# Kernel optimization log

Measured on AMD Instinct MI355X. Metric: run time of the kernel, lower is better.

## Reference

```python
import jax, jax.numpy as jnp
import numpy as np

B, D, U = 32768, 256, 256
P0, P1, NC = 128, 64, 1


def setup_inputs() -> dict:
    key = jax.random.key(0)
    ks = jax.random.split(key, 36)
    nrm = lambda k, shp, s=0.05: jax.random.normal(k, shp, jnp.float32) * s
    inp = {
        "x": jax.random.normal(ks[0], (B, D), jnp.float32),
        "click": jax.random.uniform(ks[1], (B, 1), dtype=jnp.float32),
        "h_c": jax.random.normal(ks[2], (B, U), jnp.float32),
        "h_v": jax.random.normal(ks[3], (B, U), jnp.float32),
        "s_c": jax.random.normal(ks[4], (B, U), jnp.float32),
        "s_v": jax.random.normal(ks[5], (B, U), jnp.float32),
        "g_prev": jax.random.randint(ks[6], (B, U), 0, 2).astype(jnp.int32),
        # gate weights: order [f, i, o, g]; x-gates have bias, h-gates do not
        "Wx_c": nrm(ks[7], (4, D, U)), "bx_c": nrm(ks[8], (4, U)), "Wh_c": nrm(ks[9], (4, U, U)),
        "Wx_v": nrm(ks[10], (4, D, U)), "bx_v": nrm(ks[11], (4, U)), "Wh_v": nrm(ks[12], (4, U, U)),
        "W_schat_c": nrm(ks[13], (U, U)), "W_schat_v": nrm(ks[14], (U, U)),
        "W_svhat_v": nrm(ks[15], (U, U)), "W_svhat_c": nrm(ks[16], (U, U)),
        "Wpc0": nrm(ks[17], (U, P0)), "bpc0": nrm(ks[18], (P0,)),
        "Wpc1": nrm(ks[19], (P0, P1)), "bpc1": nrm(ks[20], (P1,)),
        "Wfcc": nrm(ks[21], (P1, NC)), "bfcc": nrm(ks[22], (NC,)),
        "Wpv0": nrm(ks[23], (U, P0)), "bpv0": nrm(ks[24], (P0,)),
        "Wpv1": nrm(ks[25], (P0, P1)), "bpv1": nrm(ks[26], (P1,)),
        "Wfcv": nrm(ks[27], (P1, NC)), "bfcv": nrm(ks[28], (NC,)),
    }
    return inp


def _leaky(x):
    return jnp.where(x > 0, x, 0.3 * x)  # keras LeakyReLU default alpha=0.3


def _mlp(h, W0, b0, W1, b1, Wf, bf):
    a = _leaky(h @ W0 + b0)
    a = _leaky(a @ W1 + b1)
    return jax.nn.sigmoid(a @ Wf + bf)


def reference(x, click, h_c, h_v, s_c, s_v, g_prev,
              Wx_c, bx_c, Wh_c, Wx_v, bx_v, Wh_v,
              W_schat_c, W_schat_v, W_svhat_v, W_svhat_c,
              Wpc0, bpc0, Wpc1, bpc1, Wfcc, bfcc,
              Wpv0, bpv0, Wpv1, bpv1, Wfcv, bfcv):
    gp = g_prev > 0  # [B, U]
    # click branch
    s_c_hat = jnp.where(gp, h_v @ W_schat_v, h_c @ W_schat_c)
    pre_c = (jnp.einsum('bd,kdu->kbu', x, Wx_c) + bx_c[:, None, :]
             + jnp.einsum('bu,kuv->kbv', s_c_hat, Wh_c))  # [4, B, U]
    f_c = jax.nn.sigmoid(pre_c[0]); i_c = jax.nn.sigmoid(pre_c[1])
    o_c = jax.nn.sigmoid(pre_c[2]); g_c = jnp.tanh(pre_c[3])
    s_c_n = i_c * g_c + jnp.where(gp, 0.0, f_c * s_c)
    h_c_n = o_c * jnp.tanh(s_c_n)
    h_c_p = _mlp(h_c_n, Wpc0, bpc0, Wpc1, bpc1, Wfcc, bfcc)  # [B, 1]
    # conversion branch, gated by click label
    gm = click >= 0.5  # [B, 1] broadcasts over U (== tf.tile)
    s_v_hat = h_v @ W_svhat_v + jnp.where(gm, h_c_n @ W_svhat_c, 0.0)
    pre_v = (jnp.einsum('bd,kdu->kbu', x, Wx_v) + bx_v[:, None, :]
             + jnp.einsum('bu,kuv->kbv', s_v_hat, Wh_v))
    f_v = jax.nn.sigmoid(pre_v[0]); i_v = jax.nn.sigmoid(pre_v[1])
    o_v = jax.nn.sigmoid(pre_v[2]); g_v = jnp.tanh(pre_v[3])
    s_v_n = jnp.where(gm, f_v * s_v + i_v * g_v, s_v)
    h_v_n = jnp.where(gm, o_v * jnp.tanh(s_v_n), h_v)
    h_v_p = _mlp(h_v_n, Wpv0, bpv0, Wpv1, bpv1, Wfcv, bfcv) * h_c_p
    g_new = jnp.broadcast_to(gm.astype(jnp.float32), (x.shape[0], U))
    return h_c_p, h_v_p, h_c_n, h_v_n, s_c_n, s_v_n, g_new
```

## Files before the change

kernel.cpp:

```cpp
#include <hip/hip_runtime.h>
#include <hip/hip_bf16.h>
#include <math.h>

typedef __bf16 bf16;
typedef __bf16 bf16x8 __attribute__((ext_vector_type(8)));
typedef float  f32x4  __attribute__((ext_vector_type(4)));

#define NB 32768
#define NU 256

#define MFMA(a,b,c) __builtin_amdgcn_mfma_f32_16x16x32_bf16((a),(b),(c),0,0,0)

static __device__ __forceinline__ float sigf(float x) {
    return 1.0f / (1.0f + __expf(-x));
}

static __device__ __forceinline__ void ld16(bf16* l, const bf16* g) {
    __builtin_amdgcn_global_load_lds(
        (const __attribute__((address_space(1))) void*)g,
        (__attribute__((address_space(3))) void*)l, 16, 0, 0);
}

static __device__ __forceinline__ bf16x8 frag(const bf16* buf, int row, int hi) {
    return *reinterpret_cast<const bf16x8*>(buf + row * 32 + hi * 8);
}

__global__ void k_cvt(const float* __restrict__ x, const float* __restrict__ h_v,
                      const float* __restrict__ h_c,
                      bf16* __restrict__ xs, bf16* __restrict__ hv_cat,
                      bf16* __restrict__ hcb)
{
    const int j = blockIdx.y;
    const int gid = blockIdx.x * 256 + threadIdx.x;
    const int row = gid >> 5, col = (gid & 31) * 8;
    const float* src = (j == 0) ? x : (j == 1) ? h_v : h_c;
    bf16* dst; int stride;
    if (j == 0)      { dst = xs;     stride = 512; }
    else if (j == 1) { dst = hv_cat; stride = 512; }
    else             { dst = hcb;    stride = 256; }
    const f32x4* s4 = reinterpret_cast<const f32x4*>(src + row * 256 + col);
    const f32x4 a = s4[0], b = s4[1];
    bf16x8 o;
    o[0] = (bf16)a[0]; o[1] = (bf16)a[1]; o[2] = (bf16)a[2]; o[3] = (bf16)a[3];
    o[4] = (bf16)b[0]; o[5] = (bf16)b[1]; o[6] = (bf16)b[2]; o[7] = (bf16)b[3];
    *reinterpret_cast<bf16x8*>(dst + row * stride + col) = o;
}

struct TrJobs {
    const float* src[24];
    bf16*        dst[24];
    int R[24], C[24], dstr[24];
};

__global__ void k_tr(TrJobs J) {
    __shared__ float tile[32][33];
    const int j = blockIdx.y;
    const int R = J.R[j], C = J.C[j], dstr = J.dstr[j];
    const int tilesC = C >> 5;
    const int tr = blockIdx.x / tilesC, tc = blockIdx.x % tilesC;
    if (tr >= (R >> 5)) return;
    const int r0 = tr * 32, c0 = tc * 32;
    const int tx = threadIdx.x, ty = threadIdx.y;
    const float* src = J.src[j];
    bf16* dst = J.dst[j];
#pragma unroll
    for (int i = 0; i < 4; ++i)
        tile[ty + 8 * i][tx] = src[(r0 + ty + 8 * i) * C + c0 + tx];
    __syncthreads();
#pragma unroll
    for (int i = 0; i < 4; ++i)
        dst[(c0 + ty + 8 * i) * dstr + r0 + tx] = (bf16)tile[tx][ty + 8 * i];
}

__global__ __launch_bounds__(256) void k_schat_t(
    const bf16* __restrict__ hc, const bf16* __restrict__ hvcat,
    const bf16* __restrict__ WTc, const bf16* __restrict__ WTv,
    const int* __restrict__ g_prev, bf16* __restrict__ xs)
{
    __shared__ bf16 A1[128 * 32], A2[128 * 32], B1[64 * 32], B2[64 * 32];
    const int tid = threadIdx.x, lane = tid & 63, w = tid >> 6;
    const int lr = lane & 15, hi = lane >> 4;
    const int r0 = blockIdx.x * 128, c0 = blockIdx.y * 64;
    const int wr = w >> 1, wc = w & 1;
    const int srow = tid >> 2, skc = (tid & 3) * 8;
    f32x4 acc1[4][2] = {}, acc2[4][2] = {};
    for (int kk = 0; kk < 8; ++kk) {
        const int k0 = kk * 32;
        if (kk) __syncthreads();
        ld16(A1 + tid * 8,        hc    + (r0 + srow) * 256 + k0 + skc);
        ld16(A1 + 2048 + tid * 8, hc    + (r0 + 64 + srow) * 256 + k0 + skc);
        ld16(A2 + tid * 8,        hvcat + (r0 + srow) * 512 + k0 + skc);
        ld16(A2 + 2048 + tid * 8, hvcat + (r0 + 64 + srow) * 512 + k0 + skc);
        ld16(B1 + tid * 8,        WTc   + (c0 + srow) * 256 + k0 + skc);
        ld16(B2 + tid * 8,        WTv   + (c0 + srow) * 256 + k0 + skc);
        __syncthreads();
        bf16x8 a1[4], a2[4], b1[2], b2[2];
#pragma unroll
        for (int i = 0; i < 4; ++i) {
            a1[i] = frag(A1, wr * 64 + i * 16 + lr, hi);
            a2[i] = frag(A2, wr * 64 + i * 16 + lr, hi);
        }
#pragma unroll
        for (int jj = 0; jj < 2; ++jj) {
            b1[jj] = frag(B1, wc * 32 + jj * 16 + lr, hi);
            b2[jj] = frag(B2, wc * 32 + jj * 16 + lr, hi);
        }
#pragma unroll
        for (int i = 0; i < 4; ++i)
#pragma unroll
            for (int jj = 0; jj < 2; ++jj) {
                acc1[i][jj] = MFMA(a1[i], b1[jj], acc1[i][jj]);
                acc2[i][jj] = MFMA(a2[i], b2[jj], acc2[i][jj]);
            }
    }
#pragma unroll
    for (int i = 0; i < 4; ++i)
#pragma unroll
        for (int jj = 0; jj < 2; ++jj)
#pragma unroll
            for (int r = 0; r < 4; ++r) {
                const int row = r0 + wr * 64 + i * 16 + hi * 4 + r;
                const int col = c0 + wc * 32 + jj * 16 + lr;
                const int o = row * 256 + col;
                const float v = (g_prev[o] > 0) ? acc2[i][jj][r] : acc1[i][jj][r];
                xs[row * 512 + 256 + col] = (bf16)v;
            }
}

__global__ __launch_bounds__(256) void k_svhat_t(
    const bf16* __restrict__ hvcat, const bf16* __restrict__ Wsv,
    bf16* __restrict__ xs)
{
    __shared__ bf16 A[128 * 32], B[128 * 32];
    const int tid = threadIdx.x, lane = tid & 63, w = tid >> 6;
    const int lr = lane & 15, hi = lane >> 4;
    const int r0 = blockIdx.x * 128, c0 = blockIdx.y * 128;
    const int wr = w >> 1, wc = w & 1;
    const int srow = tid >> 2, skc = (tid & 3) * 8;
    f32x4 acc[4][4] = {};
    for (int kk = 0; kk < 16; ++kk) {
        const int k0 = kk * 32;
        if (kk) __syncthreads();
        ld16(A + tid * 8,        hvcat + (r0 + srow) * 512 + k0 + skc);
        ld16(A + 2048 + tid * 8, hvcat + (r0 + 64 + srow) * 512 + k0 + skc);
        ld16(B + tid * 8,        Wsv   + (c0 + srow) * 512 + k0 + skc);
        ld16(B + 2048 + tid * 8, Wsv   + (c0 + 64 + srow) * 512 + k0 + skc);
        __syncthreads();
        bf16x8 a[4], b[4];
#pragma unroll
        for (int i = 0; i < 4; ++i) a[i] = frag(A, wr * 64 + i * 16 + lr, hi);
#pragma unroll
        for (int jj = 0; jj < 4; ++jj) b[jj] = frag(B, wc * 64 + jj * 16 + lr, hi);
#pragma unroll
        for (int i = 0; i < 4; ++i)
#pragma unroll
            for (int jj = 0; jj < 4; ++jj)
                acc[i][jj] = MFMA(a[i], b[jj], acc[i][jj]);
    }
#pragma unroll
    for (int i = 0; i < 4; ++i)
#pragma unroll
        for (int jj = 0; jj < 4; ++jj)
#pragma unroll
            for (int r = 0; r < 4; ++r) {
                const int row = r0 + wr * 64 + i * 16 + hi * 4 + r;
                const int col = c0 + wc * 64 + jj * 16 + lr;
                xs[row * 512 + 256 + col] = (bf16)acc[i][jj][r];
            }
}

__global__ __launch_bounds__(256) void k_gates_t(
    const bf16* __restrict__ xs, const bf16* __restrict__ WgT,
    const float* __restrict__ bx, const float* __restrict__ click,
    const int* __restrict__ g_prev, const float* __restrict__ s_prev,
    const float* __restrict__ h_prev,
    float* __restrict__ out_s, float* __restrict__ out_h,
    float* __restrict__ out_g, bf16* __restrict__ hnb,
    bf16* __restrict__ hmask_dst, int mode)
{
    __shared__ bf16 A[128 * 32], B[128 * 32];
    const int tid = threadIdx.x, lane = tid & 63, w = tid >> 6;
    const int lr = lane & 15, hi = lane >> 4;
    const int r0 = blockIdx.x * 128, u0 = blockIdx.y * 32;
    const int srow = tid >> 2, skc = (tid & 3) * 8;
    f32x4 acc[2][8] = {};
    for (int kk = 0; kk < 16; ++kk) {
        const int k0 = kk * 32;
        if (kk) __syncthreads();
        ld16(A + tid * 8,        xs + (r0 + srow) * 512 + k0 + skc);
        ld16(A + 2048 + tid * 8, xs + (r0 + 64 + srow) * 512 + k0 + skc);
        {
            int nl = srow, g = nl >> 5, ul = nl & 31;
            ld16(B + tid * 8, WgT + (g * 256 + u0 + ul) * 512 + k0 + skc);
            nl = 64 + srow; g = nl >> 5; ul = nl & 31;
            ld16(B + 2048 + tid * 8, WgT + (g * 256 + u0 + ul) * 512 + k0 + skc);
        }
        __syncthreads();
        bf16x8 a[2], b[8];
#pragma unroll
        for (int i = 0; i < 2; ++i) a[i] = frag(A, w * 32 + i * 16 + lr, hi);
#pragma unroll
        for (int nb = 0; nb < 8; ++nb) b[nb] = frag(B, nb * 16 + lr, hi);
#pragma unroll
        for (int i = 0; i < 2; ++i)
#pragma unroll
            for (int nb = 0; nb < 8; ++nb)
                acc[i][nb] = MFMA(a[i], b[nb], acc[i][nb]);
    }
#pragma unroll
    for (int uh = 0; uh < 2; ++uh) {
        const int u = u0 + uh * 16 + lr;
        const float bf_ = bx[u], bi_ = bx[256 + u];
        const float bo_ = bx[512 + u], bg_ = bx[768 + u];
#pragma unroll
        for (int i = 0; i < 2; ++i)
#pragma unroll
            for (int r = 0; r < 4; ++r) {
                const int row = r0 + w * 32 + i * 16 + hi * 4 + r;
                const int o = row * 256 + u;
                const float f  = sigf(acc[i][0 + uh][r] + bf_);
                const float ii = sigf(acc[i][2 + uh][r] + bi_);
                const float oo = sigf(acc[i][4 + uh][r] + bo_);
                const float gg = tanhf(acc[i][6 + uh][r] + bg_);
                if (mode == 0) {
                    const bool gp = g_prev[o] > 0;
                    const float sn = ii * gg + (gp ? 0.0f : f * s_prev[o]);
                    const float hn = oo * tanhf(sn);
                    out_s[o] = sn;
                    out_h[o] = hn;
                    hnb[o]   = (bf16)hn;
                    hmask_dst[row * 512 + 256 + u] =
                        (click[row] >= 0.5f) ? (bf16)hn : (bf16)0.0f;
                } else {
                    const bool m = click[row] >= 0.5f;
                    const float sv = s_prev[o];
                    const float sn = m ? (f * sv + ii * gg) : sv;
                    const float hn = m ? (oo * tanhf(sn)) : h_prev[o];
                    out_s[o] = sn;
                    out_h[o] = hn;
                    out_g[o] = m ? 1.0f : 0.0f;
                    hnb[o]   = (bf16)hn;
                }
            }
    }
}

__global__ __launch_bounds__(256) void k_mlp_t(
    const bf16* __restrict__ A_, int K, int ksteps,
    const bf16* __restrict__ WT, const float* __restrict__ bias,
    bf16* __restrict__ outp, int N)
{
    __shared__ bf16 A[128 * 32], B[64 * 32];
    const int tid = threadIdx.x, lane = tid & 63, w = tid >> 6;
    const int lr = lane & 15, hi = lane >> 4;
    const int r0 = blockIdx.x * 128, c0 = blockIdx.y * 64;
    const int srow = tid >> 2, skc = (tid & 3) * 8;
    f32x4 acc[2][4] = {};
    for (int kk = 0; kk < ksteps; ++kk) {
        const int k0 = kk * 32;
        if (kk) __syncthreads();
        ld16(A + tid * 8,        A_ + (r0 + srow) * K + k0 + skc);
        ld16(A + 2048 + tid * 8, A_ + (r0 + 64 + srow) * K + k0 + skc);
        ld16(B + tid * 8,        WT + (c0 + srow) * K + k0 + skc);
        __syncthreads();
        bf16x8 a[2], b[4];
#pragma unroll
        for (int i = 0; i < 2; ++i) a[i] = frag(A, w * 32 + i * 16 + lr, hi);
#pragma unroll
        for (int jj = 0; jj < 4; ++jj) b[jj] = frag(B, jj * 16 + lr, hi);
#pragma unroll
        for (int i = 0; i < 2; ++i)
#pragma unroll
            for (int jj = 0; jj < 4; ++jj)
                acc[i][jj] = MFMA(a[i], b[jj], acc[i][jj]);
    }
#pragma unroll
    for (int i = 0; i < 2; ++i)
#pragma unroll
        for (int jj = 0; jj < 4; ++jj)
#pragma unroll
            for (int r = 0; r < 4; ++r) {
                const int row = r0 + w * 32 + i * 16 + hi * 4 + r;
                const int col = c0 + jj * 16 + lr;
                float v = acc[i][jj][r] + bias[col];
                v = v > 0.0f ? v : 0.3f * v;
                outp[row * N + col] = (bf16)v;
            }
}

__global__ void k_final(
    const bf16* __restrict__ a2, const float* __restrict__ wv,
    const float* __restrict__ bias, const float* __restrict__ scale,
    float* __restrict__ outp)
{
    const int b = blockIdx.x * blockDim.x + threadIdx.x;
    const bf16x8* rp = reinterpret_cast<const bf16x8*>(a2 + b * 64);
    float s = bias[0];
#pragma unroll
    for (int j = 0; j < 8; ++j) {
        const bf16x8 f = rp[j];
#pragma unroll
        for (int e = 0; e < 8; ++e) s += (float)f[e] * wv[j * 8 + e];
    }
    float v = sigf(s);
    if (scale) v *= scale[b];
    outp[b] = v;
}

extern "C" void kernel_launch(void* const* d_in, const int* in_sizes, int n_in,
                              void* d_out, int out_size, void* d_ws, size_t ws_size,
                              hipStream_t stream)
{
    const float* x         = (const float*)d_in[0];
    const float* click     = (const float*)d_in[1];
    const float* h_c       = (const float*)d_in[2];
    const float* h_v       = (const float*)d_in[3];
    const float* s_c       = (const float*)d_in[4];
    const float* s_v       = (const float*)d_in[5];
    const int*   g_prev    = (const int*)d_in[6];
    const float* Wx_c      = (const float*)d_in[7];
    const float* bx_c      = (const float*)d_in[8];
    const float* Wh_c      = (const float*)d_in[9];
    const float* Wx_v      = (const float*)d_in[10];
    const float* bx_v      = (const float*)d_in[11];
    const float* Wh_v      = (const float*)d_in[12];
    const float* W_schat_c = (const float*)d_in[13];
    const float* W_schat_v = (const float*)d_in[14];
    const float* W_svhat_v = (const float*)d_in[15];
    const float* W_svhat_c = (const float*)d_in[16];
    const float* Wpc0 = (const float*)d_in[17];
    const float* bpc0 = (const float*)d_in[18];
    const float* Wpc1 = (const float*)d_in[19];
    const float* bpc1 = (const float*)d_in[20];
    const float* Wfcc = (const float*)d_in[21];
    const float* bfcc = (const float*)d_in[22];
    const float* Wpv0 = (const float*)d_in[23];
    const float* bpv0 = (const float*)d_in[24];
    const float* Wpv1 = (const float*)d_in[25];
    const float* bpv1 = (const float*)d_in[26];
    const float* Wfcv = (const float*)d_in[27];
    const float* bfcv = (const float*)d_in[28];

    float* out     = (float*)d_out;
    float* out_hcp = out;
    float* out_hvp = out + NB;
    float* out_hcn = out + 2 * NB;
    float* out_hvn = out_hcn + NB * NU;
    float* out_scn = out_hvn + NB * NU;
    float* out_svn = out_scn + NB * NU;
    float* out_gnw = out_svn + NB * NU;

    bf16* w = (bf16*)d_ws;
    bf16* WTc    = w; w += 256 * 256;
    bf16* WTv    = w; w += 256 * 256;
    bf16* Wsv    = w; w += 256 * 512;
    bf16* WT_pc0 = w; w += 128 * 256;
    bf16* WT_pv0 = w; w += 128 * 256;
    bf16* WT_pc1 = w; w += 64 * 128;
    bf16* WT_pv1 = w; w += 64 * 128;
    bf16* WgT_c  = w; w += 4 * 256 * 512;
    bf16* WgT_v  = w; w += 4 * 256 * 512;
    bf16* xs     = w; w += NB * 512;
    bf16* hv_cat = w; w += NB * 512;
    bf16* buf256 = w; w += NB * 256;
    bf16* bufP0  = w; w += NB * 128;
    bf16* bufP1  = w; w += NB * 64;

    TrJobs J;
    int j = 0;
    J.src[j] = W_schat_c; J.dst[j] = WTc; J.R[j] = 256; J.C[j] = 256; J.dstr[j] = 256; ++j;
    J.src[j] = W_schat_v; J.dst[j] = WTv; J.R[j] = 256; J.C[j] = 256; J.dstr[j] = 256; ++j;
    J.src[j] = W_svhat_v; J.dst[j] = Wsv;       J.R[j] = 256; J.C[j] = 256; J.dstr[j] = 512; ++j;
    J.src[j] = W_svhat_c; J.dst[j] = Wsv + 256; J.R[j] = 256; J.C[j] = 256; J.dstr[j] = 512; ++j;
    J.src[j] = Wpc0; J.dst[j] = WT_pc0; J.R[j] = 256; J.C[j] = 128; J.dstr[j] = 256; ++j;
    J.src[j] = Wpv0; J.dst[j] = WT_pv0; J.R[j] = 256; J.C[j] = 128; J.dstr[j] = 256; ++j;
    J.src[j] = Wpc1; J.dst[j] = WT_pc1; J.R[j] = 128; J.C[j] = 64;  J.dstr[j] = 128; ++j;
    J.src[j] = Wpv1; J.dst[j] = WT_pv1; J.R[j] = 128; J.C[j] = 64;  J.dstr[j] = 128; ++j;
    for (int g = 0; g < 4; ++g) {
        J.src[j] = Wx_c + g * 65536; J.dst[j] = WgT_c + g * 131072;       J.R[j] = 256; J.C[j] = 256; J.dstr[j] = 512; ++j;
        J.src[j] = Wh_c + g * 65536; J.dst[j] = WgT_c + g * 131072 + 256; J.R[j] = 256; J.C[j] = 256; J.dstr[j] = 512; ++j;
    }
    for (int g = 0; g < 4; ++g) {
        J.src[j] = Wx_v + g * 65536; J.dst[j] = WgT_v + g * 131072;       J.R[j] = 256; J.C[j] = 256; J.dstr[j] = 512; ++j;
        J.src[j] = Wh_v + g * 65536; J.dst[j] = WgT_v + g * 131072 + 256; J.R[j] = 256; J.C[j] = 256; J.dstr[j] = 512; ++j;
    }

    k_cvt<<<dim3(4096, 3), 256, 0, stream>>>(x, h_v, h_c, xs, hv_cat, buf256);
    k_tr<<<dim3(64, 24), dim3(32, 8), 0, stream>>>(J);

    k_schat_t<<<dim3(256, 4), 256, 0, stream>>>(buf256, hv_cat, WTc, WTv, g_prev, xs);
    k_gates_t<<<dim3(256, 8), 256, 0, stream>>>(xs, WgT_c, bx_c, click, g_prev, s_c,
                                                nullptr, out_scn, out_hcn, nullptr,
                                                buf256, hv_cat, 0);
    k_mlp_t<<<dim3(256, 2), 256, 0, stream>>>(buf256, 256, 8, WT_pc0, bpc0, bufP0, 128);
    k_mlp_t<<<dim3(256, 1), 256, 0, stream>>>(bufP0, 128, 4, WT_pc1, bpc1, bufP1, 64);
    k_final<<<NB / 256, 256, 0, stream>>>(bufP1, Wfcc, bfcc, nullptr, out_hcp);

    k_svhat_t<<<dim3(256, 2), 256, 0, stream>>>(hv_cat, Wsv, xs);
    k_gates_t<<<dim3(256, 8), 256, 0, stream>>>(xs, WgT_v, bx_v, click, nullptr, s_v,
                                                h_v, out_svn, out_hvn, out_gnw,
                                                buf256, nullptr, 1);
    k_mlp_t<<<dim3(256, 2), 256, 0, stream>>>(buf256, 256, 8, WT_pv0, bpv0, bufP0, 128);
    k_mlp_t<<<dim3(256, 1), 256, 0, stream>>>(bufP0, 128, 4, WT_pv1, bpv1, bufP1, 64);
    k_final<<<NB / 256, 256, 0, stream>>>(bufP1, Wfcv, bfcv, out_hcp, out_hvp);
}
```

Before: 681.1 us.

## Fuse MLP stages, bit-pack g_prev, widen K tiles with swizzled LDS, faster activations

Replaces the two-layer MLP plus final-dot kernels with one fused kernel per branch that keeps the hidden layer in shared memory, removing the intermediate bf16 buffers and extra launches. g_prev is packed into a bitmask once, so the gating kernels read bits instead of int32 per element. GEMM kernels now stage 64-wide K tiles with an XOR-swizzled LDS layout, halving barrier count and reducing bank conflicts. sigmoid uses a hardware reciprocal and tanh is computed through sigmoid, at some precision cost.

```diff
diff --git a/kernel.cpp b/kernel.cpp
--- a/kernel.cpp
+++ b/kernel.cpp
@@ -12,7 +12,10 @@
 #define MFMA(a,b,c) __builtin_amdgcn_mfma_f32_16x16x32_bf16((a),(b),(c),0,0,0)
 
 static __device__ __forceinline__ float sigf(float x) {
-    return 1.0f / (1.0f + __expf(-x));
+    return __builtin_amdgcn_rcpf(1.0f + __expf(-x));
+}
+static __device__ __forceinline__ float tanh_(float x) {
+    return fmaf(2.0f, sigf(2.0f * x), -1.0f);
 }
 
 static __device__ __forceinline__ void ld16(bf16* l, const bf16* g) {
@@ -21,8 +24,8 @@
         (__attribute__((address_space(3))) void*)l, 16, 0, 0);
 }
 
-static __device__ __forceinline__ bf16x8 frag(const bf16* buf, int row, int hi) {
-    return *reinterpret_cast<const bf16x8*>(buf + row * 32 + hi * 8);
+static __device__ __forceinline__ bf16x8 frag64(const bf16* buf, int row, int kc) {
+    return *reinterpret_cast<const bf16x8*>(buf + row * 64 + ((kc ^ (row & 7)) * 8));
 }
 
 __global__ void k_cvt(const float* __restrict__ x, const float* __restrict__ h_v,
@@ -46,6 +49,17 @@
     *reinterpret_cast<bf16x8*>(dst + row * stride + col) = o;
 }
 
+__global__ void k_pack(const int* __restrict__ g, unsigned long long* __restrict__ m)
+{
+    const int tid0 = blockIdx.x * 256 + threadIdx.x;
+#pragma unroll
+    for (int it = 0; it < 32; ++it) {
+        const int i = tid0 + it * (1024 * 256);
+        const unsigned long long b = __ballot(g[i] > 0);
+        if ((threadIdx.x & 63) == 0) m[i >> 6] = b;
+    }
+}
+
 struct TrJobs {
     const float* src[24];
     bf16*        dst[24];
@@ -75,43 +89,53 @@
 __global__ __launch_bounds__(256) void k_schat_t(
     const bf16* __restrict__ hc, const bf16* __restrict__ hvcat,
     const bf16* __restrict__ WTc, const bf16* __restrict__ WTv,
-    const int* __restrict__ g_prev, bf16* __restrict__ xs)
-{
-    __shared__ bf16 A1[128 * 32], A2[128 * 32], B1[64 * 32], B2[64 * 32];
+    const unsigned* __restrict__ gmask, bf16* __restrict__ xs)
+{
+    __shared__ bf16 A1[128 * 64], A2[128 * 64], B1[64 * 64], B2[64 * 64];
     const int tid = threadIdx.x, lane = tid & 63, w = tid >> 6;
     const int lr = lane & 15, hi = lane >> 4;
     const int r0 = blockIdx.x * 128, c0 = blockIdx.y * 64;
     const int wr = w >> 1, wc = w & 1;
-    const int srow = tid >> 2, skc = (tid & 3) * 8;
     f32x4 acc1[4][2] = {}, acc2[4][2] = {};
-    for (int kk = 0; kk < 8; ++kk) {
-        const int k0 = kk * 32;
+    for (int kk = 0; kk < 4; ++kk) {
+        const int k0 = kk * 64;
         if (kk) __syncthreads();
-        ld16(A1 + tid * 8,        hc    + (r0 + srow) * 256 + k0 + skc);
-        ld16(A1 + 2048 + tid * 8, hc    + (r0 + 64 + srow) * 256 + k0 + skc);
-        ld16(A2 + tid * 8,        hvcat + (r0 + srow) * 512 + k0 + skc);
-        ld16(A2 + 2048 + tid * 8, hvcat + (r0 + 64 + srow) * 512 + k0 + skc);
-        ld16(B1 + tid * 8,        WTc   + (c0 + srow) * 256 + k0 + skc);
-        ld16(B2 + tid * 8,        WTv   + (c0 + srow) * 256 + k0 + skc);
-        __syncthreads();
-        bf16x8 a1[4], a2[4], b1[2], b2[2];
-#pragma unroll
-        for (int i = 0; i < 4; ++i) {
-            a1[i] = frag(A1, wr * 64 + i * 16 + lr, hi);
-            a2[i] = frag(A2, wr * 64 + i * 16 + lr, hi);
-        }
-#pragma unroll
-        for (int jj = 0; jj < 2; ++jj) {
-            b1[jj] = frag(B1, wc * 32 + jj * 16 + lr, hi);
-            b2[jj] = frag(B2, wc * 32 + jj * 16 + lr, hi);
-        }
-#pragma unroll
-        for (int i = 0; i < 4; ++i)
+#pragma unroll
+        for (int p = 0; p < 4; ++p) {
+            const int t = tid + p * 256;
+            const int row = t >> 3, gs = ((t & 7) ^ (row & 7)) * 8;
+            ld16(A1 + t * 8, hc    + (r0 + row) * 256 + k0 + gs);
+            ld16(A2 + t * 8, hvcat + (r0 + row) * 512 + k0 + gs);
+        }
+#pragma unroll
+        for (int p = 0; p < 2; ++p) {
+            const int t = tid + p * 256;
+            const int row = t >> 3, gs = ((t & 7) ^ (row & 7)) * 8;
+            ld16(B1 + t * 8, WTc + (c0 + row) * 256 + k0 + gs);
+            ld16(B2 + t * 8, WTv + (c0 + row) * 256 + k0 + gs);
+        }
+        __syncthreads();
+#pragma unroll
+        for (int ks = 0; ks < 2; ++ks) {
+            bf16x8 a1[4], a2[4], b1[2], b2[2];
+#pragma unroll
+            for (int i = 0; i < 4; ++i) {
+                a1[i] = frag64(A1, wr * 64 + i * 16 + lr, ks * 4 + hi);
+                a2[i] = frag64(A2, wr * 64 + i * 16 + lr, ks * 4 + hi);
+            }
 #pragma unroll
             for (int jj = 0; jj < 2; ++jj) {
-                acc1[i][jj] = MFMA(a1[i], b1[jj], acc1[i][jj]);
-                acc2[i][jj] = MFMA(a2[i], b2[jj], acc2[i][jj]);
+                b1[jj] = frag64(B1, wc * 32 + jj * 16 + lr, ks * 4 + hi);
+                b2[jj] = frag64(B2, wc * 32 + jj * 16 + lr, ks * 4 + hi);
             }
+#pragma unroll
+            for (int i = 0; i < 4; ++i)
+#pragma unroll
+                for (int jj = 0; jj < 2; ++jj) {
+                    acc1[i][jj] = MFMA(a1[i], b1[jj], acc1[i][jj]);
+                    acc2[i][jj] = MFMA(a2[i], b2[jj], acc2[i][jj]);
+                }
+        }
     }
 #pragma unroll
     for (int i = 0; i < 4; ++i)
@@ -121,9 +145,8 @@
             for (int r = 0; r < 4; ++r) {
                 const int row = r0 + wr * 64 + i * 16 + hi * 4 + r;
                 const int col = c0 + wc * 32 + jj * 16 + lr;
-                const int o = row * 256 + col;
-                const float v = (g_prev[o] > 0) ? acc2[i][jj][r] : acc1[i][jj][r];
-                xs[row * 512 + 256 + col] = (bf16)v;
+                const bool gp = (gmask[row * 8 + (col >> 5)] >> (col & 31)) & 1;
+                xs[row * 512 + 256 + col] = (bf16)(gp ? acc2[i][jj][r] : acc1[i][jj][r]);
             }
 }
 
@@ -131,31 +154,36 @@
     const bf16* __restrict__ hvcat, const bf16* __restrict__ Wsv,
     bf16* __restrict__ xs)
 {
-    __shared__ bf16 A[128 * 32], B[128 * 32];
+    __shared__ bf16 A[128 * 64], B[128 * 64];
     const int tid = threadIdx.x, lane = tid & 63, w = tid >> 6;
     const int lr = lane & 15, hi = lane >> 4;
     const int r0 = blockIdx.x * 128, c0 = blockIdx.y * 128;
     const int wr = w >> 1, wc = w & 1;
-    const int srow = tid >> 2, skc = (tid & 3) * 8;
     f32x4 acc[4][4] = {};
-    for (int kk = 0; kk < 16; ++kk) {
-        const int k0 = kk * 32;
+    for (int kk = 0; kk < 8; ++kk) {
+        const int k0 = kk * 64;
         if (kk) __syncthreads();
-        ld16(A + tid * 8,        hvcat + (r0 + srow) * 512 + k0 + skc);
-        ld16(A + 2048 + tid * 8, hvcat + (r0 + 64 + srow) * 512 + k0 + skc);
-        ld16(B + tid * 8,        Wsv   + (c0 + srow) * 512 + k0 + skc);
-        ld16(B + 2048 + tid * 8, Wsv   + (c0 + 64 + srow) * 512 + k0 + skc);
-        __syncthreads();
-        bf16x8 a[4], b[4];
-#pragma unroll
-        for (int i = 0; i < 4; ++i) a[i] = frag(A, wr * 64 + i * 16 + lr, hi);
-#pragma unroll
-        for (int jj = 0; jj < 4; ++jj) b[jj] = frag(B, wc * 64 + jj * 16 + lr, hi);
-#pragma unroll
-        for (int i = 0; i < 4; ++i)
-#pragma unroll
-            for (int jj = 0; jj < 4; ++jj)
-                acc[i][jj] = MFMA(a[i], b[jj], acc[i][jj]);
+#pragma unroll
+        for (int p = 0; p < 4; ++p) {
+            const int t = tid + p * 256;
+            const int row = t >> 3, gs = ((t & 7) ^ (row & 7)) * 8;
+            ld16(A + t * 8, hvcat + (r0 + row) * 512 + k0 + gs);
+            ld16(B + t * 8, Wsv   + (c0 + row) * 512 + k0 + gs);
+        }
+        __syncthreads();
+#pragma unroll
+        for (int ks = 0; ks < 2; ++ks) {
+            bf16x8 a[4], b[4];
+#pragma unroll
+            for (int i = 0; i < 4; ++i) a[i] = frag64(A, wr * 64 + i * 16 + lr, ks * 4 + hi);
+#pragma unroll
+            for (int jj = 0; jj < 4; ++jj) b[jj] = frag64(B, wc * 64 + jj * 16 + lr, ks * 4 + hi);
+#pragma unroll
+            for (int i = 0; i < 4; ++i)
+#pragma unroll
+                for (int jj = 0; jj < 4; ++jj)
+                    acc[i][jj] = MFMA(a[i], b[jj], acc[i][jj]);
+        }
     }
 #pragma unroll
     for (int i = 0; i < 4; ++i)
@@ -172,139 +200,192 @@
 __global__ __launch_bounds__(256) void k_gates_t(
     const bf16* __restrict__ xs, const bf16* __restrict__ WgT,
     const float* __restrict__ bx, const float* __restrict__ click,
-    const int* __restrict__ g_prev, const float* __restrict__ s_prev,
+    const unsigned* __restrict__ gmask, const float* __restrict__ s_prev,
     const float* __restrict__ h_prev,
     float* __restrict__ out_s, float* __restrict__ out_h,
     float* __restrict__ out_g, bf16* __restrict__ hnb,
     bf16* __restrict__ hmask_dst, int mode)
 {
-    __shared__ bf16 A[128 * 32], B[128 * 32];
+    __shared__ bf16 A[128 * 64], B[128 * 64];
     const int tid = threadIdx.x, lane = tid & 63, w = tid >> 6;
     const int lr = lane & 15, hi = lane >> 4;
     const int r0 = blockIdx.x * 128, u0 = blockIdx.y * 32;
-    const int srow = tid >> 2, skc = (tid & 3) * 8;
     f32x4 acc[2][8] = {};
-    for (int kk = 0; kk < 16; ++kk) {
-        const int k0 = kk * 32;
+    for (int kk = 0; kk < 8; ++kk) {
+        const int k0 = kk * 64;
         if (kk) __syncthreads();
-        ld16(A + tid * 8,        xs + (r0 + srow) * 512 + k0 + skc);
-        ld16(A + 2048 + tid * 8, xs + (r0 + 64 + srow) * 512 + k0 + skc);
-        {
-            int nl = srow, g = nl >> 5, ul = nl & 31;
-            ld16(B + tid * 8, WgT + (g * 256 + u0 + ul) * 512 + k0 + skc);
-            nl = 64 + srow; g = nl >> 5; ul = nl & 31;
-            ld16(B + 2048 + tid * 8, WgT + (g * 256 + u0 + ul) * 512 + k0 + skc);
-        }
-        __syncthreads();
-        bf16x8 a[2], b[8];
-#pragma unroll
-        for (int i = 0; i < 2; ++i) a[i] = frag(A, w * 32 + i * 16 + lr, hi);
-#pragma unroll
-        for (int nb = 0; nb < 8; ++nb) b[nb] = frag(B, nb * 16 + lr, hi);
-#pragma unroll
-        for (int i = 0; i < 2; ++i)
-#pragma unroll
-            for (int nb = 0; nb < 8; ++nb)
-                acc[i][nb] = MFMA(a[i], b[nb], acc[i][nb]);
-    }
+#pragma unroll
+        for (int p = 0; p < 4; ++p) {
+            const int t = tid + p * 256;
+            const int row = t >> 3, gs = ((t & 7) ^ (row & 7)) * 8;
+            ld16(A + t * 8, xs + (r0 + row) * 512 + k0 + gs);
+            const int g = row >> 5, ul = row & 31;
+            ld16(B + t * 8, WgT + (g * 256 + u0 + ul) * 512 + k0 + gs);
+        }
+        __syncthreads();
+#pragma unroll
+        for (int ks = 0; ks < 2; ++ks) {
+            bf16x8 a[2], b[8];
+#pragma unroll
+            for (int i = 0; i < 2; ++i) a[i] = frag64(A, w * 32 + i * 16 + lr, ks * 4 + hi);
+#pragma unroll
+            for (int nb = 0; nb < 8; ++nb) b[nb] = frag64(B, nb * 16 + lr, ks * 4 + hi);
+#pragma unroll
+            for (int i = 0; i < 2; ++i)
+#pragma unroll
+                for (int nb = 0; nb < 8; ++nb)
+                    acc[i][nb] = MFMA(a[i], b[nb], acc[i][nb]);
+        }
+    }
+    const int u0b = u0 >> 5;
+    float bfv[2], biv[2], bov[2], bgv[2];
 #pragma unroll
     for (int uh = 0; uh < 2; ++uh) {
         const int u = u0 + uh * 16 + lr;
-        const float bf_ = bx[u], bi_ = bx[256 + u];
-        const float bo_ = bx[512 + u], bg_ = bx[768 + u];
-#pragma unroll
-        for (int i = 0; i < 2; ++i)
-#pragma unroll
-            for (int r = 0; r < 4; ++r) {
-                const int row = r0 + w * 32 + i * 16 + hi * 4 + r;
+        bfv[uh] = bx[u];       biv[uh] = bx[256 + u];
+        bov[uh] = bx[512 + u]; bgv[uh] = bx[768 + u];
+    }
+#pragma unroll
+    for (int i = 0; i < 2; ++i)
+#pragma unroll
+        for (int r = 0; r < 4; ++r) {
+            const int row = r0 + w * 32 + i * 16 + hi * 4 + r;
+            const float ck = click[row];
+            const unsigned mw = (mode == 0) ? gmask[row * 8 + u0b] : 0u;
+#pragma unroll
+            for (int uh = 0; uh < 2; ++uh) {
+                const int u = u0 + uh * 16 + lr;
                 const int o = row * 256 + u;
-                const float f  = sigf(acc[i][0 + uh][r] + bf_);
-                const float ii = sigf(acc[i][2 + uh][r] + bi_);
-                const float oo = sigf(acc[i][4 + uh][r] + bo_);
-                const float gg = tanhf(acc[i][6 + uh][r] + bg_);
+                const float f  = sigf(acc[i][0 + uh][r] + bfv[uh]);
+                const float ii = sigf(acc[i][2 + uh][r] + biv[uh]);
+                const float oo = sigf(acc[i][4 + uh][r] + bov[uh]);
+                const float gg = tanh_(acc[i][6 + uh][r] + bgv[uh]);
                 if (mode == 0) {
-                    const bool gp = g_prev[o] > 0;
+                    const bool gp = (mw >> (u & 31)) & 1;
                     const float sn = ii * gg + (gp ? 0.0f : f * s_prev[o]);
-                    const float hn = oo * tanhf(sn);
+                    const float hn = oo * tanh_(sn);
                     out_s[o] = sn;
                     out_h[o] = hn;
                     hnb[o]   = (bf16)hn;
                     hmask_dst[row * 512 + 256 + u] =
-                        (click[row] >= 0.5f) ? (bf16)hn : (bf16)0.0f;
+                        (ck >= 0.5f) ? (bf16)hn : (bf16)0.0f;
                 } else {
-                    const bool m = click[row] >= 0.5f;
+                    const bool m = ck >= 0.5f;
                     const float sv = s_prev[o];
                     const float sn = m ? (f * sv + ii * gg) : sv;
-                    const float hn = m ? (oo * tanhf(sn)) : h_prev[o];
+                    const float hn = m ? (oo * tanh_(sn)) : h_prev[o];
                     out_s[o] = sn;
                     out_h[o] = hn;
                     out_g[o] = m ? 1.0f : 0.0f;
                     hnb[o]   = (bf16)hn;
                 }
             }
-    }
-}
-
-__global__ __launch_bounds__(256) void k_mlp_t(
-    const bf16* __restrict__ A_, int K, int ksteps,
-    const bf16* __restrict__ WT, const float* __restrict__ bias,
-    bf16* __restrict__ outp, int N)
-{
-    __shared__ bf16 A[128 * 32], B[64 * 32];
+        }
+}
+
+__global__ __launch_bounds__(256) void k_mlp_f(
+    const bf16* __restrict__ Hin,
+    const bf16* __restrict__ WT0,
+    const float* __restrict__ b0,
+    const bf16* __restrict__ WT1,
+    const float* __restrict__ b1,
+    const float* __restrict__ wf,
+    const float* __restrict__ bf_,
+    const float* __restrict__ scale,
+    float* __restrict__ outp)
+{
+    __shared__ bf16 A[64 * 64], Bb[128 * 64], H1[64 * 128];
     const int tid = threadIdx.x, lane = tid & 63, w = tid >> 6;
     const int lr = lane & 15, hi = lane >> 4;
-    const int r0 = blockIdx.x * 128, c0 = blockIdx.y * 64;
-    const int srow = tid >> 2, skc = (tid & 3) * 8;
-    f32x4 acc[2][4] = {};
-    for (int kk = 0; kk < ksteps; ++kk) {
-        const int k0 = kk * 32;
+    const int r0 = blockIdx.x * 64;
+    f32x4 acc[8] = {};
+    for (int kk = 0; kk < 4; ++kk) {
+        const int k0 = kk * 64;
         if (kk) __syncthreads();
-        ld16(A + tid * 8,        A_ + (r0 + srow) * K + k0 + skc);
-        ld16(A + 2048 + tid * 8, A_ + (r0 + 64 + srow) * K + k0 + skc);
-        ld16(B + tid * 8,        WT + (c0 + srow) * K + k0 + skc);
-        __syncthreads();
-        bf16x8 a[2], b[4];
-#pragma unroll
-        for (int i = 0; i < 2; ++i) a[i] = frag(A, w * 32 + i * 16 + lr, hi);
-#pragma unroll
-        for (int jj = 0; jj < 4; ++jj) b[jj] = frag(B, jj * 16 + lr, hi);
-#pragma unroll
-        for (int i = 0; i < 2; ++i)
-#pragma unroll
-            for (int jj = 0; jj < 4; ++jj)
-                acc[i][jj] = MFMA(a[i], b[jj], acc[i][jj]);
-    }
-#pragma unroll
-    for (int i = 0; i < 2; ++i)
-#pragma unroll
-        for (int jj = 0; jj < 4; ++jj)
-#pragma unroll
-            for (int r = 0; r < 4; ++r) {
-                const int row = r0 + w * 32 + i * 16 + hi * 4 + r;
-                const int col = c0 + jj * 16 + lr;
-                float v = acc[i][jj][r] + bias[col];
-                v = v > 0.0f ? v : 0.3f * v;
-                outp[row * N + col] = (bf16)v;
-            }
-}
-
-__global__ void k_final(
-    const bf16* __restrict__ a2, const float* __restrict__ wv,
-    const float* __restrict__ bias, const float* __restrict__ scale,
-    float* __restrict__ outp)
-{
-    const int b = blockIdx.x * blockDim.x + threadIdx.x;
-    const bf16x8* rp = reinterpret_cast<const bf16x8*>(a2 + b * 64);
-    float s = bias[0];
-#pragma unroll
-    for (int j = 0; j < 8; ++j) {
-        const bf16x8 f = rp[j];
-#pragma unroll
-        for (int e = 0; e < 8; ++e) s += (float)f[e] * wv[j * 8 + e];
-    }
-    float v = sigf(s);
-    if (scale) v *= scale[b];
-    outp[b] = v;
+#pragma unroll
+        for (int p = 0; p < 2; ++p) {
+            const int t = tid + p * 256;
+            const int row = t >> 3, gs = ((t & 7) ^ (row & 7)) * 8;
+            ld16(A + t * 8, Hin + (r0 + row) * 256 + k0 + gs);
+        }
+#pragma unroll
+        for (int p = 0; p < 4; ++p) {
+            const int t = tid + p * 256;
+            const int row = t >> 3, gs = ((t & 7) ^ (row & 7)) * 8;
+            ld16(Bb + t * 8, WT0 + row * 256 + k0 + gs);
+        }
+        __syncthreads();
+#pragma unroll
+        for (int ks = 0; ks < 2; ++ks) {
+            const bf16x8 a = frag64(A, w * 16 + lr, ks * 4 + hi);
+            bf16x8 b[8];
+#pragma unroll
+            for (int nb = 0; nb < 8; ++nb) b[nb] = frag64(Bb, nb * 16 + lr, ks * 4 + hi);
+#pragma unroll
+            for (int nb = 0; nb < 8; ++nb) acc[nb] = MFMA(a, b[nb], acc[nb]);
+        }
+    }
+#pragma unroll
+    for (int nb = 0; nb < 8; ++nb) {
+        const int col = nb * 16 + lr;
+        const float bb = b0[col];
+#pragma unroll
+        for (int r = 0; r < 4; ++r) {
+            const int rl = w * 16 + hi * 4 + r;
+            float v = acc[nb][r] + bb;
+            v = v > 0.0f ? v : 0.3f * v;
+            H1[rl * 128 + (((col >> 3) ^ (rl & 7)) * 8) + (col & 7)] = (bf16)v;
+        }
+    }
+    __syncthreads();
+    f32x4 acc2[4] = {};
+    for (int kk = 0; kk < 2; ++kk) {
+#pragma unroll
+        for (int p = 0; p < 2; ++p) {
+            const int t = tid + p * 256;
+            const int row = t >> 3, gs = ((t & 7) ^ (row & 7)) * 8;
+            ld16(Bb + t * 8, WT1 + row * 128 + kk * 64 + gs);
+        }
+        __syncthreads();
+#pragma unroll
+        for (int ks = 0; ks < 2; ++ks) {
+            const int rl = w * 16 + lr;
+            const int c = kk * 8 + ks * 4 + hi;
+            const bf16x8 a = *reinterpret_cast<const bf16x8*>(
+                H1 + rl * 128 + ((c ^ (rl & 7)) * 8));
+            bf16x8 b[4];
+#pragma unroll
+            for (int jj = 0; jj < 4; ++jj) b[jj] = frag64(Bb, jj * 16 + lr, ks * 4 + hi);
+#pragma unroll
+            for (int jj = 0; jj < 4; ++jj) acc2[jj] = MFMA(a, b[jj], acc2[jj]);
+        }
+        __syncthreads();
+    }
+    float b1v[4], wfv[4];
+#pragma unroll
+    for (int jj = 0; jj < 4; ++jj) {
+        b1v[jj] = b1[jj * 16 + lr];
+        wfv[jj] = wf[jj * 16 + lr];
+    }
+    const float bfv = bf_[0];
+#pragma unroll
+    for (int r = 0; r < 4; ++r) {
+        float p = 0.0f;
+#pragma unroll
+        for (int jj = 0; jj < 4; ++jj) {
+            float v = acc2[jj][r] + b1v[jj];
+            v = v > 0.0f ? v : 0.3f * v;
+            p = fmaf(v, wfv[jj], p);
+        }
+        p += __shfl_xor(p, 1); p += __shfl_xor(p, 2);
+        p += __shfl_xor(p, 4); p += __shfl_xor(p, 8);
+        if (lr == 0) {
+            const int row = r0 + w * 16 + hi * 4 + r;
+            float res = sigf(p + bfv);
+            if (scale) res *= scale[row];
+            outp[row] = res;
+        }
+    }
 }
 
 extern "C" void kernel_launch(void* const* d_in, const int* in_sizes, int n_in,
@@ -350,7 +431,9 @@
     float* out_svn = out_scn + NB * NU;
     float* out_gnw = out_svn + NB * NU;
 
-    bf16* w = (bf16*)d_ws;
+    unsigned long long* gmask64 = (unsigned long long*)d_ws;
+    const unsigned* gmask32 = (const unsigned*)d_ws;
+    bf16* w = (bf16*)d_ws + 524288;
     bf16* WTc    = w; w += 256 * 256;
     bf16* WTv    = w; w += 256 * 256;
     bf16* Wsv    = w; w += 256 * 512;
@@ -363,8 +446,6 @@
     bf16* xs     = w; w += NB * 512;
     bf16* hv_cat = w; w += NB * 512;
     bf16* buf256 = w; w += NB * 256;
-    bf16* bufP0  = w; w += NB * 128;
-    bf16* bufP1  = w; w += NB * 64;
 
     TrJobs J;
     int j = 0;
@@ -386,21 +467,20 @@
     }
 
     k_cvt<<<dim3(4096, 3), 256, 0, stream>>>(x, h_v, h_c, xs, hv_cat, buf256);
+    k_pack<<<1024, 256, 0, stream>>>(g_prev, gmask64);
     k_tr<<<dim3(64, 24), dim3(32, 8), 0, stream>>>(J);
 
-    k_schat_t<<<dim3(256, 4), 256, 0, stream>>>(buf256, hv_cat, WTc, WTv, g_prev, xs);
-    k_gates_t<<<dim3(256, 8), 256, 0, stream>>>(xs, WgT_c, bx_c, click, g_prev, s_c,
+    k_schat_t<<<dim3(256, 4), 256, 0, stream>>>(buf256, hv_cat, WTc, WTv, gmask32, xs);
+    k_gates_t<<<dim3(256, 8), 256, 0, stream>>>(xs, WgT_c, bx_c, click, gmask32, s_c,
                                                 nullptr, out_scn, out_hcn, nullptr,
                                                 buf256, hv_cat, 0);
-    k_mlp_t<<<dim3(256, 2), 256, 0, stream>>>(buf256, 256, 8, WT_pc0, bpc0, bufP0, 128);
-    k_mlp_t<<<dim3(256, 1), 256, 0, stream>>>(bufP0, 128, 4, WT_pc1, bpc1, bufP1, 64);
-    k_final<<<NB / 256, 256, 0, stream>>>(bufP1, Wfcc, bfcc, nullptr, out_hcp);
+    k_mlp_f<<<512, 256, 0, stream>>>(buf256, WT_pc0, bpc0, WT_pc1, bpc1,
+                                     Wfcc, bfcc, nullptr, out_hcp);
 
     k_svhat_t<<<dim3(256, 2), 256, 0, stream>>>(hv_cat, Wsv, xs);
-    k_gates_t<<<dim3(256, 8), 256, 0, stream>>>(xs, WgT_v, bx_v, click, nullptr, s_v,
+    k_gates_t<<<dim3(256, 8), 256, 0, stream>>>(xs, WgT_v, bx_v, click, gmask32, s_v,
                                                 h_v, out_svn, out_hvn, out_gnw,
                                                 buf256, nullptr, 1);
-    k_mlp_t<<<dim3(256, 2), 256, 0, stream>>>(buf256, 256, 8, WT_pv0, bpv0, bufP0, 128);
-    k_mlp_t<<<dim3(256, 1), 256, 0, stream>>>(bufP0, 128, 4, WT_pv1, bpv1, bufP1, 64);
-    k_final<<<NB / 256, 256, 0, stream>>>(bufP1, Wfcv, bfcv, out_hcp, out_hvp);
-}
+    k_mlp_f<<<512, 256, 0, stream>>>(buf256, WT_pv0, bpv0, WT_pv1, bpv1,
+                                     Wfcv, bfcv, out_hcp, out_hvp);
+}
```

Measured after the change: 586.5 us. 1.16x faster.
